# Optimization experiments

Measured on AMD Instinct MI355X. Metric: run time of the kernel, lower is better.

The kernel has to match this reference:

```python
import jax, jax.numpy as jnp
import numpy as np


def _combine(left, right):
    # complex mult-add combine: (a_r, x_r) o (a_l, x_l) = (a_r*a_l, a_r*x_l + x_r)
    alr, ali, xlr, xli = left
    arr, ari, xrr, xri = right
    rar = arr * alr - ari * ali
    rai = arr * ali + ari * alr
    rxr = arr * xlr - ari * xli + xrr
    rxi = arr * xli + ari * xlr + xri
    return (rar, rai, rxr, rxi)


def setup_inputs() -> dict:
    key = jax.random.key(0)
    k1, k2, k3, k4 = jax.random.split(key, 4)
    B, L, D = 8, 4096, 256
    A_re = jax.random.uniform(k1, (B, L, D), dtype=jnp.float32)  # |a|<1-ish for stability
    A_im = jax.random.normal(k2, (B, L, D), dtype=jnp.float32) * 0.1
    X_re = jax.random.normal(k3, (B, L, D), dtype=jnp.float32)
    X_im = jax.random.normal(k4, (B, L, D), dtype=jnp.float32)
    return {"A_re": A_re, "A_im": A_im, "X_re": X_re, "X_im": X_im}


def reference(A_re, A_im, X_re, X_im):
    # Inclusive scan of y_t = a_t * y_{t-1} + x_t (complex), over time axis 1.
    _, _, yr, yi = jax.lax.associative_scan(_combine, (A_re, A_im, X_re, X_im), axis=1)
    # [B, L, D, 2] real/imag stacked (equivalent of torch.view_as_real of the complex output)
    return jnp.stack([yr, yi], axis=-1)
```

## Files before the change

### kernel.cpp

```cpp
#include <hip/hip_runtime.h>

#define BATCH 8
#define SEQ   4096
#define DIM   256

typedef float floatx4 __attribute__((ext_vector_type(4)));


template <int NT, int T, int G>
__global__ __launch_bounds__(256) void k_tile_agg(
    const float* __restrict__ Ar, const float* __restrict__ Ai,
    const float* __restrict__ Xr, const float* __restrict__ Xi,
    float4* __restrict__ agg)
{
    int wave = threadIdx.x >> 6;
    int lane = threadIdx.x & 63;
    int tile = blockIdx.x * 4 + wave;
    int b = tile / NT;
    int j = tile - b * NT;
    int d = lane * 4;

    size_t base = ((size_t)b * SEQ + (size_t)j * T) * DIM + d;

    float ar[4], ai[4], xr[4], xi[4];
#pragma unroll
    for (int k = 0; k < 4; ++k) { ar[k] = 1.f; ai[k] = 0.f; xr[k] = 0.f; xi[k] = 0.f; }

    for (int t0 = 0; t0 < T; t0 += G) {
        float4 Lar[G], Lai[G], Lxr[G], Lxi[G];
#pragma unroll
        for (int g = 0; g < G; ++g) {
            size_t idx = base + (size_t)(t0 + g) * DIM;
            Lar[g] = *(const float4*)(Ar + idx);
            Lai[g] = *(const float4*)(Ai + idx);
            Lxr[g] = *(const float4*)(Xr + idx);
            Lxi[g] = *(const float4*)(Xi + idx);
        }
#pragma unroll
        for (int g = 0; g < G; ++g) {
            const float* pab = (const float*)&Lar[g];
            const float* pai = (const float*)&Lai[g];
            const float* pxr = (const float*)&Lxr[g];
            const float* pxi = (const float*)&Lxi[g];
#pragma unroll
            for (int k = 0; k < 4; ++k) {
                float a_r = pab[k], a_i = pai[k], x_r = pxr[k], x_i = pxi[k];
                float nar = a_r * ar[k] - a_i * ai[k];
                float nai = a_r * ai[k] + a_i * ar[k];
                float nxr = a_r * xr[k] - a_i * xi[k] + x_r;
                float nxi = a_r * xi[k] + a_i * xr[k] + x_i;
                ar[k] = nar; ai[k] = nai; xr[k] = nxr; xi[k] = nxi;
            }
        }
    }
    size_t o = ((size_t)b * NT + j) * DIM + d;
#pragma unroll
    for (int k = 0; k < 4; ++k)
        agg[o + k] = make_float4(ar[k], ai[k], xr[k], xi[k]);
}

template <int NT>
__global__ __launch_bounds__(256) void k_scan_agg(float4* __restrict__ agg)
{
    constexpr int NTPL = NT / 64;
    int lane = threadIdx.x & 63;
    int col  = blockIdx.x * 4 + (threadIdx.x >> 6);
    int b = col >> 8;
    int d = col & 255;

    float4 v[NTPL];
    float lar = 1.f, lai = 0.f, lxr = 0.f, lxi = 0.f;
#pragma unroll
    for (int m = 0; m < NTPL; ++m) {
        v[m] = agg[((size_t)b * NT + lane * NTPL + m) * DIM + d];
        float nar = v[m].x * lar - v[m].y * lai;
        float nai = v[m].x * lai + v[m].y * lar;
        float nxr = v[m].x * lxr - v[m].y * lxi + v[m].z;
        float nxi = v[m].x * lxi + v[m].y * lxr + v[m].w;
        lar = nar; lai = nai; lxr = nxr; lxi = nxi;
    }

    float ar = lar, ai = lai, xr = lxr, xi = lxi;
#pragma unroll
    for (int off = 1; off < 64; off <<= 1) {
        float par = __shfl_up(ar, (unsigned)off, 64);
        float pai = __shfl_up(ai, (unsigned)off, 64);
        float pxr = __shfl_up(xr, (unsigned)off, 64);
        float pxi = __shfl_up(xi, (unsigned)off, 64);
        if (lane >= off) {
            float nar = ar * par - ai * pai;
            float nai = ar * pai + ai * par;
            float nxr = ar * pxr - ai * pxi + xr;
            float nxi = ar * pxi + ai * pxr + xi;
            ar = nar; ai = nai; xr = nxr; xi = nxi;
        }
    }

    float ear = __shfl_up(ar, 1u, 64);
    float eai = __shfl_up(ai, 1u, 64);
    float exr = __shfl_up(xr, 1u, 64);
    float exi = __shfl_up(xi, 1u, 64);
    if (lane == 0) { ear = 1.f; eai = 0.f; exr = 0.f; exi = 0.f; }

#pragma unroll
    for (int m = 0; m < NTPL; ++m) {
        agg[((size_t)b * NT + lane * NTPL + m) * DIM + d] =
            make_float4(exr, exi, 0.f, 0.f);
        float nar = v[m].x * ear - v[m].y * eai;
        float nai = v[m].x * eai + v[m].y * ear;
        float nxr = v[m].x * exr - v[m].y * exi + v[m].z;
        float nxi = v[m].x * exi + v[m].y * exr + v[m].w;
        ear = nar; eai = nai; exr = nxr; exi = nxi;
    }
}

template <int NT, int T, int G>
__global__ __launch_bounds__(256) void k_apply(
    const float* __restrict__ Ar, const float* __restrict__ Ai,
    const float* __restrict__ Xr, const float* __restrict__ Xi,
    const float4* __restrict__ agg, float* __restrict__ outf)
{
    int wave = threadIdx.x >> 6;
    int lane = threadIdx.x & 63;
    int tile = blockIdx.x * 4 + wave;
    int b = tile / NT;
    int j = tile - b * NT;
    int d = lane * 4;

    float yr[4], yi[4];
    size_t o = ((size_t)b * NT + j) * DIM + d;
#pragma unroll
    for (int k = 0; k < 4; ++k) {
        float4 p = agg[o + k];
        yr[k] = p.x; yi[k] = p.y;
    }

    size_t base = ((size_t)b * SEQ + (size_t)j * T) * DIM + d;
    for (int t0 = 0; t0 < T; t0 += G) {
        float4 Lar[G], Lai[G], Lxr[G], Lxi[G];
#pragma unroll
        for (int g = 0; g < G; ++g) {
            size_t idx = base + (size_t)(t0 + g) * DIM;
            Lar[g] = *(const float4*)(Ar + idx);
            Lai[g] = *(const float4*)(Ai + idx);
            Lxr[g] = *(const float4*)(Xr + idx);
            Lxi[g] = *(const float4*)(Xi + idx);
        }
#pragma unroll
        for (int g = 0; g < G; ++g) {
            const float* pab = (const float*)&Lar[g];
            const float* pai = (const float*)&Lai[g];
            const float* pxr = (const float*)&Lxr[g];
            const float* pxi = (const float*)&Lxi[g];
#pragma unroll
            for (int k = 0; k < 4; ++k) {
                float nyr = pab[k] * yr[k] - pai[k] * yi[k] + pxr[k];
                float nyi = pab[k] * yi[k] + pai[k] * yr[k] + pxi[k];
                yr[k] = nyr; yi[k] = nyi;
            }
            size_t idx = base + (size_t)(t0 + g) * DIM;
            floatx4 o1 = (floatx4){yr[0], yi[0], yr[1], yi[1]};
            floatx4 o2 = (floatx4){yr[2], yi[2], yr[3], yi[3]};
            float* po = outf + 2 * idx;
            __builtin_nontemporal_store(o1, (floatx4*)(po));
            __builtin_nontemporal_store(o2, (floatx4*)(po + 4));
        }
    }
}

extern "C" void kernel_launch(void* const* d_in, const int* in_sizes, int n_in,
                              void* d_out, int out_size, void* d_ws, size_t ws_size,
                              hipStream_t stream)
{
    const float* Ar = (const float*)d_in[0];
    const float* Ai = (const float*)d_in[1];
    const float* Xr = (const float*)d_in[2];
    const float* Xi = (const float*)d_in[3];
    float* outf = (float*)d_out;
    float4* agg = (float4*)d_ws;

    dim3 block(256);

    if (ws_size >= (size_t)BATCH * 256 * DIM * sizeof(float4)) {
        constexpr int NT = 256, T = SEQ / 256;
        dim3 grid1((BATCH * NT) / 4);
        k_tile_agg<NT, T, 4><<<grid1, block, 0, stream>>>(Ar, Ai, Xr, Xi, agg);
        k_scan_agg<NT><<<(BATCH * DIM) / 4, block, 0, stream>>>(agg);
        k_apply<NT, T, 4><<<grid1, block, 0, stream>>>(Ar, Ai, Xr, Xi, agg, outf);
    } else {
        constexpr int NT = 64, T = SEQ / 64;
        dim3 grid1((BATCH * NT) / 4);
        k_tile_agg<NT, T, 4><<<grid1, block, 0, stream>>>(Ar, Ai, Xr, Xi, agg);
        k_scan_agg<NT><<<(BATCH * DIM) / 4, block, 0, stream>>>(agg);
        k_apply<NT, T, 4><<<grid1, block, 0, stream>>>(Ar, Ai, Xr, Xi, agg, outf);
    }
}
```

Baseline: 71.74 us.

## Double-buffer register loads and add finer 512-tile decomposition path

```diff
diff --git a/kernel.cpp b/kernel.cpp
--- a/kernel.cpp
+++ b/kernel.cpp
@@ -8,11 +8,12 @@
 
 
 template <int NT, int T, int G>
-__global__ __launch_bounds__(256) void k_tile_agg(
+__global__ __launch_bounds__(256, 4) void k_tile_agg(
     const float* __restrict__ Ar, const float* __restrict__ Ai,
     const float* __restrict__ Xr, const float* __restrict__ Xi,
     float4* __restrict__ agg)
 {
+    constexpr int NS = T / G;
     int wave = threadIdx.x >> 6;
     int lane = threadIdx.x & 63;
     int tile = blockIdx.x * 4 + wave;
@@ -26,22 +27,25 @@
 #pragma unroll
     for (int k = 0; k < 4; ++k) { ar[k] = 1.f; ai[k] = 0.f; xr[k] = 0.f; xi[k] = 0.f; }
 
-    for (int t0 = 0; t0 < T; t0 += G) {
-        float4 Lar[G], Lai[G], Lxr[G], Lxi[G];
+    float4 P0[4][G], P1[4][G];
+
+    auto LOAD = [&](float4 (&B)[4][G], int t0) {
 #pragma unroll
         for (int g = 0; g < G; ++g) {
             size_t idx = base + (size_t)(t0 + g) * DIM;
-            Lar[g] = *(const float4*)(Ar + idx);
-            Lai[g] = *(const float4*)(Ai + idx);
-            Lxr[g] = *(const float4*)(Xr + idx);
-            Lxi[g] = *(const float4*)(Xi + idx);
-        }
-#pragma unroll
-        for (int g = 0; g < G; ++g) {
-            const float* pab = (const float*)&Lar[g];
-            const float* pai = (const float*)&Lai[g];
-            const float* pxr = (const float*)&Lxr[g];
-            const float* pxi = (const float*)&Lxi[g];
+            B[0][g] = *(const float4*)(Ar + idx);
+            B[1][g] = *(const float4*)(Ai + idx);
+            B[2][g] = *(const float4*)(Xr + idx);
+            B[3][g] = *(const float4*)(Xi + idx);
+        }
+    };
+    auto STEP = [&](float4 (&B)[4][G]) {
+#pragma unroll
+        for (int g = 0; g < G; ++g) {
+            const float* pab = (const float*)&B[0][g];
+            const float* pai = (const float*)&B[1][g];
+            const float* pxr = (const float*)&B[2][g];
+            const float* pxi = (const float*)&B[3][g];
 #pragma unroll
             for (int k = 0; k < 4; ++k) {
                 float a_r = pab[k], a_i = pai[k], x_r = pxr[k], x_i = pxi[k];
@@ -52,7 +56,20 @@
                 ar[k] = nar; ai[k] = nai; xr[k] = nxr; xi[k] = nxi;
             }
         }
-    }
+    };
+
+    LOAD(P0, 0);
+#pragma unroll
+    for (int s = 0; s < NS; ++s) {
+        if ((s & 1) == 0) {
+            if (s + 1 < NS) LOAD(P1, (s + 1) * G);
+            STEP(P0);
+        } else {
+            if (s + 1 < NS) LOAD(P0, (s + 1) * G);
+            STEP(P1);
+        }
+    }
+
     size_t o = ((size_t)b * NT + j) * DIM + d;
 #pragma unroll
     for (int k = 0; k < 4; ++k)
@@ -115,11 +132,12 @@
 }
 
 template <int NT, int T, int G>
-__global__ __launch_bounds__(256) void k_apply(
+__global__ __launch_bounds__(256, 4) void k_apply(
     const float* __restrict__ Ar, const float* __restrict__ Ai,
     const float* __restrict__ Xr, const float* __restrict__ Xi,
     const float4* __restrict__ agg, float* __restrict__ outf)
 {
+    constexpr int NS = T / G;
     int wave = threadIdx.x >> 6;
     int lane = threadIdx.x & 63;
     int tile = blockIdx.x * 4 + wave;
@@ -136,22 +154,26 @@
     }
 
     size_t base = ((size_t)b * SEQ + (size_t)j * T) * DIM + d;
-    for (int t0 = 0; t0 < T; t0 += G) {
-        float4 Lar[G], Lai[G], Lxr[G], Lxi[G];
+
+    float4 P0[4][G], P1[4][G];
+
+    auto LOAD = [&](float4 (&B)[4][G], int t0) {
 #pragma unroll
         for (int g = 0; g < G; ++g) {
             size_t idx = base + (size_t)(t0 + g) * DIM;
-            Lar[g] = *(const float4*)(Ar + idx);
-            Lai[g] = *(const float4*)(Ai + idx);
-            Lxr[g] = *(const float4*)(Xr + idx);
-            Lxi[g] = *(const float4*)(Xi + idx);
-        }
-#pragma unroll
-        for (int g = 0; g < G; ++g) {
-            const float* pab = (const float*)&Lar[g];
-            const float* pai = (const float*)&Lai[g];
-            const float* pxr = (const float*)&Lxr[g];
-            const float* pxi = (const float*)&Lxi[g];
+            B[0][g] = *(const float4*)(Ar + idx);
+            B[1][g] = *(const float4*)(Ai + idx);
+            B[2][g] = *(const float4*)(Xr + idx);
+            B[3][g] = *(const float4*)(Xi + idx);
+        }
+    };
+    auto STEP = [&](float4 (&B)[4][G], int t0) {
+#pragma unroll
+        for (int g = 0; g < G; ++g) {
+            const float* pab = (const float*)&B[0][g];
+            const float* pai = (const float*)&B[1][g];
+            const float* pxr = (const float*)&B[2][g];
+            const float* pxi = (const float*)&B[3][g];
 #pragma unroll
             for (int k = 0; k < 4; ++k) {
                 float nyr = pab[k] * yr[k] - pai[k] * yi[k] + pxr[k];
@@ -165,6 +187,18 @@
             __builtin_nontemporal_store(o1, (floatx4*)(po));
             __builtin_nontemporal_store(o2, (floatx4*)(po + 4));
         }
+    };
+
+    LOAD(P0, 0);
+#pragma unroll
+    for (int s = 0; s < NS; ++s) {
+        if ((s & 1) == 0) {
+            if (s + 1 < NS) LOAD(P1, (s + 1) * G);
+            STEP(P0, s * G);
+        } else {
+            if (s + 1 < NS) LOAD(P0, (s + 1) * G);
+            STEP(P1, s * G);
+        }
     }
 }
 
@@ -181,17 +215,23 @@
 
     dim3 block(256);
 
-    if (ws_size >= (size_t)BATCH * 256 * DIM * sizeof(float4)) {
+    if (ws_size >= (size_t)BATCH * 512 * DIM * sizeof(float4)) {
+        constexpr int NT = 512, T = SEQ / 512;
+        dim3 grid1((BATCH * NT) / 4);
+        k_tile_agg<NT, T, 2><<<grid1, block, 0, stream>>>(Ar, Ai, Xr, Xi, agg);
+        k_scan_agg<NT><<<(BATCH * DIM) / 4, block, 0, stream>>>(agg);
+        k_apply<NT, T, 2><<<grid1, block, 0, stream>>>(Ar, Ai, Xr, Xi, agg, outf);
+    } else if (ws_size >= (size_t)BATCH * 256 * DIM * sizeof(float4)) {
         constexpr int NT = 256, T = SEQ / 256;
         dim3 grid1((BATCH * NT) / 4);
-        k_tile_agg<NT, T, 4><<<grid1, block, 0, stream>>>(Ar, Ai, Xr, Xi, agg);
+        k_tile_agg<NT, T, 2><<<grid1, block, 0, stream>>>(Ar, Ai, Xr, Xi, agg);
         k_scan_agg<NT><<<(BATCH * DIM) / 4, block, 0, stream>>>(agg);
-        k_apply<NT, T, 4><<<grid1, block, 0, stream>>>(Ar, Ai, Xr, Xi, agg, outf);
+        k_apply<NT, T, 2><<<grid1, block, 0, stream>>>(Ar, Ai, Xr, Xi, agg, outf);
     } else {
         constexpr int NT = 64, T = SEQ / 64;
         dim3 grid1((BATCH * NT) / 4);
-        k_tile_agg<NT, T, 4><<<grid1, block, 0, stream>>>(Ar, Ai, Xr, Xi, agg);
+        k_tile_agg<NT, T, 2><<<grid1, block, 0, stream>>>(Ar, Ai, Xr, Xi, agg);
         k_scan_agg<NT><<<(BATCH * DIM) / 4, block, 0, stream>>>(agg);
-        k_apply<NT, T, 4><<<grid1, block, 0, stream>>>(Ar, Ai, Xr, Xi, agg, outf);
-    }
-}
+        k_apply<NT, T, 2><<<grid1, block, 0, stream>>>(Ar, Ai, Xr, Xi, agg, outf);
+    }
+}
```

Result: slower. 83.53 us (+16.4%).
